# Performance work log

Hardware: AMD Instinct MI355X
Metric: run time of the kernel (lower is better)

The kernel has to match this reference:

```python
import jax, jax.numpy as jnp
import numpy as np

G, D, H, O = 8, 1024, 2048, 1024

def _xavier(key, shape):
    # xavier_normal_ on nn.Linear weight [out, in]: std = sqrt(2/(fan_in+fan_out))
    fan_out, fan_in = shape[-2], shape[-1]
    std = float(np.sqrt(2.0 / (fan_in + fan_out)))
    return jax.random.normal(key, shape, dtype=jnp.float32) * std

def setup_inputs() -> dict:
    key = jax.random.key(0)
    kx, kg, ku, kd = jax.random.split(key, 4)
    x = jax.random.normal(kx, (65536, D), dtype=jnp.float32)
    # weights stored per-group in nn.Linear layout [out, in]
    Wg = _xavier(kg, (G, H, D))
    Wu = _xavier(ku, (G, H, D))
    Wd = _xavier(kd, (G, O, H))
    return {"x": x, "Wg": Wg, "Wu": Wu, "Wd": Wd}

def reference(x, Wg, Wu, Wd):
    # x: [B*G, D] -> [B, G, D]
    xb = x.reshape(-1, G, D)
    gate = jnp.einsum('bgd,ghd->bgh', xb, Wg)   # [B, G, H]
    up = jnp.einsum('bgd,ghd->bgh', xb, Wu)     # [B, G, H]
    hidden = jax.nn.silu(gate) * up             # fused SwiGLU
    out = jnp.einsum('bgh,goh->bgo', hidden, Wd)  # [B, G, O]
    return out.reshape(-1, O)
```

## Files before the change

### kernel.cpp

```cpp
#include <hip/hip_runtime.h>


#define GN 8
#define DN 1024
#define HN 2048
#define ON 1024
#define BN 8192

typedef __attribute__((ext_vector_type(8))) short short8;
typedef __attribute__((ext_vector_type(4))) float f32x4;
typedef __attribute__((ext_vector_type(4))) unsigned int u32x4;

__device__ __forceinline__ void async16(const void* g, void* l) {
  __builtin_amdgcn_global_load_lds(
      (const __attribute__((address_space(1))) void*)g,
      (__attribute__((address_space(3))) void*)l, 16, 0, 0);
}

__device__ __forceinline__ unsigned short f2bf(float f) {
  unsigned int u = __float_as_uint(f);
  u += 0x7FFFu + ((u >> 16) & 1u);
  return (unsigned short)(u >> 16);
}

__global__ __launch_bounds__(256) void cvt_f32_bf16(
    const float* __restrict__ in, unsigned short* __restrict__ out, int n) {
  int t = blockIdx.x * 256 + threadIdx.x;
  int i = t * 8;
  if (i >= n) return;
  f32x4 a = *(const f32x4*)(in + i);
  f32x4 b = *(const f32x4*)(in + i + 4);
  u32x4 r;
  r.x = (unsigned)f2bf(a.x) | ((unsigned)f2bf(a.y) << 16);
  r.y = (unsigned)f2bf(a.z) | ((unsigned)f2bf(a.w) << 16);
  r.z = (unsigned)f2bf(b.x) | ((unsigned)f2bf(b.y) << 16);
  r.w = (unsigned)f2bf(b.z) | ((unsigned)f2bf(b.w) << 16);
  *(u32x4*)(out + i) = r;
}

__global__ __launch_bounds__(256, 2) void gemm1_swiglu(
    const unsigned short* __restrict__ Xb, const unsigned short* __restrict__ Wgb,
    const unsigned short* __restrict__ Wub, unsigned short* __restrict__ Hid) {
  const int g = blockIdx.z;
  const int m0 = blockIdx.x * 128;
  const int n0 = blockIdx.y * 64;
  const int tid = threadIdx.x;
  const int lane = tid & 63;
  const int w = tid >> 6;
  const int wm = w >> 1, wn = w & 1;

  __shared__ __align__(16) unsigned short lA[128 * 64];
  __shared__ __align__(16) unsigned short lG[64 * 64];
  __shared__ __align__(16) unsigned short lU[64 * 64];

  const int rl = lane >> 3;
  const int gc = (lane & 7) ^ rl;

  const unsigned short* aptr[4];
#pragma unroll
  for (int i = 0; i < 4; ++i) {
    int r = w * 32 + i * 8 + rl;
    aptr[i] = Xb + ((size_t)((m0 + r) * 8 + g)) * DN + gc * 8;
  }
  const unsigned short *gptr[2], *uptr[2];
#pragma unroll
  for (int i = 0; i < 2; ++i) {
    int r = w * 16 + i * 8 + rl;
    gptr[i] = Wgb + ((size_t)(g * HN + n0 + r)) * DN + gc * 8;
    uptr[i] = Wub + ((size_t)(g * HN + n0 + r)) * DN + gc * 8;
  }

  f32x4 accg[4][2], accu[4][2];
#pragma unroll
  for (int mi = 0; mi < 4; ++mi)
#pragma unroll
    for (int ni = 0; ni < 2; ++ni) {
      accg[mi][ni] = (f32x4)(0.0f);
      accu[mi][ni] = (f32x4)(0.0f);
    }

  for (int k0 = 0; k0 < DN; k0 += 64) {
#pragma unroll
    for (int i = 0; i < 4; ++i)
      async16(aptr[i] + k0, &lA[(w * 32 + i * 8) * 64]);
#pragma unroll
    for (int i = 0; i < 2; ++i) {
      async16(gptr[i] + k0, &lG[(w * 16 + i * 8) * 64]);
      async16(uptr[i] + k0, &lU[(w * 16 + i * 8) * 64]);
    }
    __syncthreads();

#pragma unroll
    for (int ks = 0; ks < 2; ++ks) {
      const int c = (lane >> 4) + ks * 4;
      short8 af[4], bg[2], bu[2];
#pragma unroll
      for (int mi = 0; mi < 4; ++mi) {
        int r = wm * 64 + mi * 16 + (lane & 15);
        af[mi] = *(const short8*)&lA[r * 64 + ((c ^ (r & 7)) * 8)];
      }
#pragma unroll
      for (int ni = 0; ni < 2; ++ni) {
        int r = wn * 32 + ni * 16 + (lane & 15);
        int off = r * 64 + ((c ^ (r & 7)) * 8);
        bg[ni] = *(const short8*)&lG[off];
        bu[ni] = *(const short8*)&lU[off];
      }
#pragma unroll
      for (int mi = 0; mi < 4; ++mi)
#pragma unroll
        for (int ni = 0; ni < 2; ++ni) {
          accg[mi][ni] = __builtin_amdgcn_mfma_f32_16x16x32_bf16(
              af[mi], bg[ni], accg[mi][ni], 0, 0, 0);
          accu[mi][ni] = __builtin_amdgcn_mfma_f32_16x16x32_bf16(
              af[mi], bu[ni], accu[mi][ni], 0, 0, 0);
        }
    }
    __syncthreads();
  }

  const int q = lane >> 4, cl = lane & 15;
#pragma unroll
  for (int mi = 0; mi < 4; ++mi)
#pragma unroll
    for (int ni = 0; ni < 2; ++ni) {
      int hcol = n0 + wn * 32 + ni * 16 + cl;
#pragma unroll
      for (int i = 0; i < 4; ++i) {
        int b = m0 + wm * 64 + mi * 16 + q * 4 + i;
        float gf = accg[mi][ni][i];
        float uf = accu[mi][ni][i];
        float hv = (gf / (1.0f + __expf(-gf))) * uf;
        Hid[((size_t)(b * 8 + g)) * HN + hcol] = f2bf(hv);
      }
    }
}

__global__ __launch_bounds__(256, 2) void gemm2_down(
    const unsigned short* __restrict__ Hid, const unsigned short* __restrict__ Wdb,
    float* __restrict__ Out) {
  const int g = blockIdx.z;
  const int m0 = blockIdx.x * 128;
  const int n0 = blockIdx.y * 128;
  const int tid = threadIdx.x;
  const int lane = tid & 63;
  const int w = tid >> 6;
  const int wm = w >> 1, wn = w & 1;

  __shared__ __align__(16) unsigned short lA[128 * 64];
  __shared__ __align__(16) unsigned short lB[128 * 64];

  const int rl = lane >> 3;
  const int gc = (lane & 7) ^ rl;

  const unsigned short *aptr[4], *bptr[4];
#pragma unroll
  for (int i = 0; i < 4; ++i) {
    int r = w * 32 + i * 8 + rl;
    aptr[i] = Hid + ((size_t)((m0 + r) * 8 + g)) * HN + gc * 8;
    bptr[i] = Wdb + ((size_t)(g * ON + n0 + r)) * HN + gc * 8;
  }

  f32x4 acc[4][4];
#pragma unroll
  for (int mi = 0; mi < 4; ++mi)
#pragma unroll
    for (int ni = 0; ni < 4; ++ni) acc[mi][ni] = (f32x4)(0.0f);

  for (int k0 = 0; k0 < HN; k0 += 64) {
#pragma unroll
    for (int i = 0; i < 4; ++i) {
      async16(aptr[i] + k0, &lA[(w * 32 + i * 8) * 64]);
      async16(bptr[i] + k0, &lB[(w * 32 + i * 8) * 64]);
    }
    __syncthreads();

#pragma unroll
    for (int ks = 0; ks < 2; ++ks) {
      const int c = (lane >> 4) + ks * 4;
      short8 af[4], bf[4];
#pragma unroll
      for (int mi = 0; mi < 4; ++mi) {
        int r = wm * 64 + mi * 16 + (lane & 15);
        af[mi] = *(const short8*)&lA[r * 64 + ((c ^ (r & 7)) * 8)];
      }
#pragma unroll
      for (int ni = 0; ni < 4; ++ni) {
        int r = wn * 64 + ni * 16 + (lane & 15);
        bf[ni] = *(const short8*)&lB[r * 64 + ((c ^ (r & 7)) * 8)];
      }
#pragma unroll
      for (int mi = 0; mi < 4; ++mi)
#pragma unroll
        for (int ni = 0; ni < 4; ++ni)
          acc[mi][ni] = __builtin_amdgcn_mfma_f32_16x16x32_bf16(
              af[mi], bf[ni], acc[mi][ni], 0, 0, 0);
    }
    __syncthreads();
  }

  const int q = lane >> 4, cl = lane & 15;
#pragma unroll
  for (int mi = 0; mi < 4; ++mi)
#pragma unroll
    for (int ni = 0; ni < 4; ++ni) {
      int o = n0 + wn * 64 + ni * 16 + cl;
#pragma unroll
      for (int i = 0; i < 4; ++i) {
        int b = m0 + wm * 64 + mi * 16 + q * 4 + i;
        Out[((size_t)(b * 8 + g)) * ON + o] = acc[mi][ni][i];
      }
    }
}

extern "C" void kernel_launch(void* const* d_in, const int* in_sizes, int n_in,
                              void* d_out, int out_size, void* d_ws, size_t ws_size,
                              hipStream_t stream) {
  const float* x  = (const float*)d_in[0];
  const float* Wg = (const float*)d_in[1];
  const float* Wu = (const float*)d_in[2];
  const float* Wd = (const float*)d_in[3];
  float* out = (float*)d_out;

  const int NX = 65536 * 1024;
  const int NW = GN * HN * DN;

  unsigned short* xb = (unsigned short*)d_ws;
  unsigned short* wg = xb + (size_t)NX;
  unsigned short* wu = wg + (size_t)NW;
  unsigned short* wd = wu + (size_t)NW;
  unsigned short* hid = wd + (size_t)NW;

  cvt_f32_bf16<<<NX / 8 / 256, 256, 0, stream>>>(x, xb, NX);
  cvt_f32_bf16<<<NW / 8 / 256, 256, 0, stream>>>(Wg, wg, NW);
  cvt_f32_bf16<<<NW / 8 / 256, 256, 0, stream>>>(Wu, wu, NW);
  cvt_f32_bf16<<<NW / 8 / 256, 256, 0, stream>>>(Wd, wd, NW);

  gemm1_swiglu<<<dim3(BN / 128, HN / 64, GN), 256, 0, stream>>>(xb, wg, wu, hid);

  gemm2_down<<<dim3(BN / 128, ON / 128, GN), 256, 0, stream>>>(hid, wd, out);
}
```

Before: 1.438 ms.

## Rewrite both GEMMs as 256-tile, 8-wave, multi-buffered pipelined MFMA kernels

Both grouped GEMM kernels move to 512-thread blocks with larger 256-row tiles (256x128 for gate/up, 256x256 for down) and a 128 KB dynamic-LDS four-slot buffer split into K halves. Async global-to-LDS loads are interleaved with MFMA phases under explicit vmcnt waits, barriers and raised wave priority. A 1D grid with an XCD-aware block swizzle improves L2 reuse. The aim is to hide load latency and raise arithmetic intensity per LDS byte, at the cost of more registers per thread and heavy reliance on fragile hand-tuned waitcnt accounting.

```diff
diff --git a/kernel.cpp b/kernel.cpp
--- a/kernel.cpp
+++ b/kernel.cpp
@@ -5,11 +5,13 @@
 #define DN 1024
 #define HN 2048
 #define ON 1024
-#define BN 8192
 
 typedef __attribute__((ext_vector_type(8))) short short8;
 typedef __attribute__((ext_vector_type(4))) float f32x4;
 typedef __attribute__((ext_vector_type(4))) unsigned int u32x4;
+
+#define SBAR() __builtin_amdgcn_sched_barrier(0)
+#define BARR() __builtin_amdgcn_s_barrier()
 
 __device__ __forceinline__ void async16(const void* g, void* l) {
   __builtin_amdgcn_global_load_lds(
@@ -38,177 +40,309 @@
   *(u32x4*)(out + i) = r;
 }
 
-__global__ __launch_bounds__(256, 2) void gemm1_swiglu(
+__global__ __launch_bounds__(512, 2) void gemm1_swiglu(
     const unsigned short* __restrict__ Xb, const unsigned short* __restrict__ Wgb,
     const unsigned short* __restrict__ Wub, unsigned short* __restrict__ Hid) {
-  const int g = blockIdx.z;
-  const int m0 = blockIdx.x * 128;
-  const int n0 = blockIdx.y * 64;
+  extern __shared__ unsigned short sm[];
+  unsigned short* sA = sm;
+  unsigned short* sG = sm + 32768;
+  unsigned short* sU = sm + 49152;
+
+  const int bid = blockIdx.x;
+  const int swz = (bid & 7) * 512 + (bid >> 3);
+  const int g = swz >> 9;
+  const int rem = swz & 511;
+  const int m0 = (rem >> 4) * 256;
+  const int n0 = (rem & 15) * 128;
+
   const int tid = threadIdx.x;
   const int lane = tid & 63;
   const int w = tid >> 6;
-  const int wm = w >> 1, wn = w & 1;
-
-  __shared__ __align__(16) unsigned short lA[128 * 64];
-  __shared__ __align__(16) unsigned short lG[64 * 64];
-  __shared__ __align__(16) unsigned short lU[64 * 64];
-
-  const int rl = lane >> 3;
-  const int gc = (lane & 7) ^ rl;
-
-  const unsigned short* aptr[4];
-#pragma unroll
-  for (int i = 0; i < 4; ++i) {
-    int r = w * 32 + i * 8 + rl;
-    aptr[i] = Xb + ((size_t)((m0 + r) * 8 + g)) * DN + gc * 8;
-  }
-  const unsigned short *gptr[2], *uptr[2];
-#pragma unroll
-  for (int i = 0; i < 2; ++i) {
-    int r = w * 16 + i * 8 + rl;
-    gptr[i] = Wgb + ((size_t)(g * HN + n0 + r)) * DN + gc * 8;
-    uptr[i] = Wub + ((size_t)(g * HN + n0 + r)) * DN + gc * 8;
-  }
-
-  f32x4 accg[4][2], accu[4][2];
-#pragma unroll
-  for (int mi = 0; mi < 4; ++mi)
+  const int wm = w >> 2, wn = w & 3;
+  const int fr = lane & 15, fc = lane >> 4;
+  const int sR = (fc + ((fr >> 1) & 3)) & 3;
+
+  const unsigned short* aSrc[2];
+  unsigned short* aDst[2];
+#pragma unroll
+  for (int j = 0; j < 2; ++j) {
+    int R = j * 128 + w * 16 + (lane >> 2);
+    int c = ((lane & 3) - ((R >> 1) & 3)) & 3;
+    aSrc[j] = Xb + ((size_t)((m0 + R) * 8 + g)) * DN + c * 8;
+    aDst[j] = &sA[(j * 128 + w * 16) * 32];
+  }
+  const unsigned short *gSrc, *uSrc;
+  unsigned short *gDst, *uDst;
+  {
+    int R = w * 16 + (lane >> 2);
+    int c = ((lane & 3) - ((R >> 1) & 3)) & 3;
+    gSrc = Wgb + ((size_t)(g * HN + n0 + R)) * DN + c * 8;
+    uSrc = Wub + ((size_t)(g * HN + n0 + R)) * DN + c * 8;
+    gDst = &sG[(w * 16) * 32];
+    uDst = &sU[(w * 16) * 32];
+  }
+
+  auto stageA = [&](int t, int kk) {
+    const int buf = (t & 1) * 2 + kk;
+    const int ko = t * 64 + kk * 32;
+#pragma unroll
+    for (int j = 0; j < 2; ++j) async16(aSrc[j] + ko, aDst[j] + buf * 8192);
+  };
+  auto stageB = [&](int t, int kk) {
+    const int buf = (t & 1) * 2 + kk;
+    const int ko = t * 64 + kk * 32;
+    async16(gSrc + ko, gDst + buf * 4096);
+    async16(uSrc + ko, uDst + buf * 4096);
+  };
+  auto readA = [&](int t, int kk, short8* a) {
+    const unsigned short* p =
+        sA + ((t & 1) * 2 + kk) * 8192 + (wm * 128 + fr) * 32 + sR * 8;
+#pragma unroll
+    for (int mi = 0; mi < 8; ++mi) a[mi] = *(const short8*)(p + mi * 512);
+  };
+  auto readB = [&](const unsigned short* base, int t, int kk, short8* b) {
+    const unsigned short* p =
+        base + ((t & 1) * 2 + kk) * 4096 + (wn * 32 + fr) * 32 + sR * 8;
+#pragma unroll
+    for (int ni = 0; ni < 2; ++ni) b[ni] = *(const short8*)(p + ni * 512);
+  };
+
+  f32x4 accg[8][2], accu[8][2];
+#pragma unroll
+  for (int mi = 0; mi < 8; ++mi)
 #pragma unroll
     for (int ni = 0; ni < 2; ++ni) {
       accg[mi][ni] = (f32x4)(0.0f);
       accu[mi][ni] = (f32x4)(0.0f);
     }
 
-  for (int k0 = 0; k0 < DN; k0 += 64) {
-#pragma unroll
-    for (int i = 0; i < 4; ++i)
-      async16(aptr[i] + k0, &lA[(w * 32 + i * 8) * 64]);
-#pragma unroll
-    for (int i = 0; i < 2; ++i) {
-      async16(gptr[i] + k0, &lG[(w * 16 + i * 8) * 64]);
-      async16(uptr[i] + k0, &lU[(w * 16 + i * 8) * 64]);
-    }
-    __syncthreads();
-
-#pragma unroll
-    for (int ks = 0; ks < 2; ++ks) {
-      const int c = (lane >> 4) + ks * 4;
-      short8 af[4], bg[2], bu[2];
-#pragma unroll
-      for (int mi = 0; mi < 4; ++mi) {
-        int r = wm * 64 + mi * 16 + (lane & 15);
-        af[mi] = *(const short8*)&lA[r * 64 + ((c ^ (r & 7)) * 8)];
-      }
-#pragma unroll
-      for (int ni = 0; ni < 2; ++ni) {
-        int r = wn * 32 + ni * 16 + (lane & 15);
-        int off = r * 64 + ((c ^ (r & 7)) * 8);
-        bg[ni] = *(const short8*)&lG[off];
-        bu[ni] = *(const short8*)&lU[off];
-      }
-#pragma unroll
-      for (int mi = 0; mi < 4; ++mi)
-#pragma unroll
-        for (int ni = 0; ni < 2; ++ni) {
-          accg[mi][ni] = __builtin_amdgcn_mfma_f32_16x16x32_bf16(
-              af[mi], bg[ni], accg[mi][ni], 0, 0, 0);
-          accu[mi][ni] = __builtin_amdgcn_mfma_f32_16x16x32_bf16(
-              af[mi], bu[ni], accu[mi][ni], 0, 0, 0);
-        }
-    }
-    __syncthreads();
+  auto mm16 = [&](const short8* a, const short8* b, f32x4(*acc)[2]) {
+    __builtin_amdgcn_s_setprio(1);
+#pragma unroll
+    for (int mi = 0; mi < 8; ++mi)
+#pragma unroll
+      for (int ni = 0; ni < 2; ++ni)
+        acc[mi][ni] = __builtin_amdgcn_mfma_f32_16x16x32_bf16(
+            a[mi], b[ni], acc[mi][ni], 0, 0, 0);
+    __builtin_amdgcn_s_setprio(0);
+  };
+
+  stageA(0, 0); stageB(0, 0); stageA(0, 1); stageB(0, 1);
+  stageA(1, 0); stageB(1, 0); stageA(1, 1);
+  asm volatile("s_waitcnt vmcnt(6)" ::: "memory");
+  SBAR(); BARR(); SBAR();
+
+  short8 af[8], bg[2], bu[2];
+  const int NIT = DN / 128;
+#pragma unroll 1
+  for (int i = 0; i < NIT; ++i) {
+    const int T = 2 * i;
+    const bool full = (i + 1 < NIT);
+    readA(T, 0, af); readB(sG, T, 0, bg);
+    stageB(T + 1, 1);
+    SBAR(); BARR(); SBAR();
+    mm16(af, bg, accg);
+    SBAR(); BARR(); SBAR();
+    readB(sU, T, 0, bu);
+    if (full) stageA(T + 2, 0);
+    SBAR(); BARR(); SBAR();
+    mm16(af, bu, accu);
+    SBAR(); BARR(); SBAR();
+    readA(T, 1, af); readB(sG, T, 1, bg);
+    if (full) stageB(T + 2, 0);
+    SBAR(); BARR(); SBAR();
+    mm16(af, bg, accg);
+    SBAR(); BARR(); SBAR();
+    readB(sU, T, 1, bu);
+    if (full) stageA(T + 2, 1);
+    SBAR(); BARR(); SBAR();
+    mm16(af, bu, accu);
+    if (full) { asm volatile("s_waitcnt vmcnt(6)" ::: "memory"); }
+    else      { asm volatile("s_waitcnt vmcnt(0)" ::: "memory"); }
+    SBAR(); BARR(); SBAR();
+    readA(T + 1, 0, af); readB(sG, T + 1, 0, bg);
+    if (full) stageB(T + 2, 1);
+    SBAR(); BARR(); SBAR();
+    mm16(af, bg, accg);
+    SBAR(); BARR(); SBAR();
+    readB(sU, T + 1, 0, bu);
+    if (full) stageA(T + 3, 0);
+    SBAR(); BARR(); SBAR();
+    mm16(af, bu, accu);
+    SBAR(); BARR(); SBAR();
+    readA(T + 1, 1, af); readB(sG, T + 1, 1, bg);
+    if (full) stageB(T + 3, 0);
+    SBAR(); BARR(); SBAR();
+    mm16(af, bg, accg);
+    SBAR(); BARR(); SBAR();
+    readB(sU, T + 1, 1, bu);
+    if (full) stageA(T + 3, 1);
+    SBAR(); BARR(); SBAR();
+    mm16(af, bu, accu);
+    if (full) { asm volatile("s_waitcnt vmcnt(6)" ::: "memory"); }
+    SBAR(); BARR(); SBAR();
   }
 
   const int q = lane >> 4, cl = lane & 15;
 #pragma unroll
-  for (int mi = 0; mi < 4; ++mi)
+  for (int mi = 0; mi < 8; ++mi)
 #pragma unroll
     for (int ni = 0; ni < 2; ++ni) {
       int hcol = n0 + wn * 32 + ni * 16 + cl;
 #pragma unroll
-      for (int i = 0; i < 4; ++i) {
-        int b = m0 + wm * 64 + mi * 16 + q * 4 + i;
-        float gf = accg[mi][ni][i];
-        float uf = accu[mi][ni][i];
+      for (int i2 = 0; i2 < 4; ++i2) {
+        int b = m0 + wm * 128 + mi * 16 + q * 4 + i2;
+        float gf = accg[mi][ni][i2];
+        float uf = accu[mi][ni][i2];
         float hv = (gf / (1.0f + __expf(-gf))) * uf;
         Hid[((size_t)(b * 8 + g)) * HN + hcol] = f2bf(hv);
       }
     }
 }
 
-__global__ __launch_bounds__(256, 2) void gemm2_down(
+__global__ __launch_bounds__(512, 2) void gemm2_down(
     const unsigned short* __restrict__ Hid, const unsigned short* __restrict__ Wdb,
     float* __restrict__ Out) {
-  const int g = blockIdx.z;
-  const int m0 = blockIdx.x * 128;
-  const int n0 = blockIdx.y * 128;
+  extern __shared__ unsigned short sm[];
+  unsigned short* sA = sm;
+  unsigned short* sB = sm + 32768;
+
+  const int bid = blockIdx.x;
+  const int swz = (bid & 7) * 128 + (bid >> 3);
+  const int g = swz >> 7;
+  const int rem = swz & 127;
+  const int m0 = (rem >> 2) * 256;
+  const int n0 = (rem & 3) * 256;
+
   const int tid = threadIdx.x;
   const int lane = tid & 63;
   const int w = tid >> 6;
-  const int wm = w >> 1, wn = w & 1;
-
-  __shared__ __align__(16) unsigned short lA[128 * 64];
-  __shared__ __align__(16) unsigned short lB[128 * 64];
-
-  const int rl = lane >> 3;
-  const int gc = (lane & 7) ^ rl;
-
-  const unsigned short *aptr[4], *bptr[4];
-#pragma unroll
-  for (int i = 0; i < 4; ++i) {
-    int r = w * 32 + i * 8 + rl;
-    aptr[i] = Hid + ((size_t)((m0 + r) * 8 + g)) * HN + gc * 8;
-    bptr[i] = Wdb + ((size_t)(g * ON + n0 + r)) * HN + gc * 8;
-  }
-
-  f32x4 acc[4][4];
-#pragma unroll
-  for (int mi = 0; mi < 4; ++mi)
+  const int wm = w >> 2, wn = w & 3;
+  const int fr = lane & 15, fc = lane >> 4;
+  const int sR = (fc + ((fr >> 1) & 3)) & 3;
+
+  const unsigned short* aSrc[2];
+  const unsigned short* bSrc[2];
+  unsigned short* aDst[2];
+  unsigned short* bDst[2];
+#pragma unroll
+  for (int j = 0; j < 2; ++j) {
+    int R = j * 128 + w * 16 + (lane >> 2);
+    int c = ((lane & 3) - ((R >> 1) & 3)) & 3;
+    aSrc[j] = Hid + ((size_t)((m0 + R) * 8 + g)) * HN + c * 8;
+    bSrc[j] = Wdb + ((size_t)(g * ON + n0 + R)) * HN + c * 8;
+    aDst[j] = &sA[(j * 128 + w * 16) * 32];
+    bDst[j] = &sB[(j * 128 + w * 16) * 32];
+  }
+
+  auto stageA = [&](int t, int kk) {
+    const int buf = (t & 1) * 2 + kk;
+    const int ko = t * 64 + kk * 32;
+#pragma unroll
+    for (int j = 0; j < 2; ++j) async16(aSrc[j] + ko, aDst[j] + buf * 8192);
+  };
+  auto stageB = [&](int t, int kk) {
+    const int buf = (t & 1) * 2 + kk;
+    const int ko = t * 64 + kk * 32;
+#pragma unroll
+    for (int j = 0; j < 2; ++j) async16(bSrc[j] + ko, bDst[j] + buf * 8192);
+  };
+  auto readA = [&](int t, int kk, short8* a) {
+    const unsigned short* p =
+        sA + ((t & 1) * 2 + kk) * 8192 + (wm * 128 + fr) * 32 + sR * 8;
+#pragma unroll
+    for (int mi = 0; mi < 8; ++mi) a[mi] = *(const short8*)(p + mi * 512);
+  };
+  auto readB = [&](int t, int kk, int nb, short8* b) {
+    const unsigned short* p =
+        sB + ((t & 1) * 2 + kk) * 8192 + (wn * 64 + nb * 16 + fr) * 32 + sR * 8;
+#pragma unroll
+    for (int nj = 0; nj < 2; ++nj) b[nj] = *(const short8*)(p + nj * 512);
+  };
+
+  f32x4 acc[8][4];
+#pragma unroll
+  for (int mi = 0; mi < 8; ++mi)
 #pragma unroll
     for (int ni = 0; ni < 4; ++ni) acc[mi][ni] = (f32x4)(0.0f);
 
-  for (int k0 = 0; k0 < HN; k0 += 64) {
-#pragma unroll
-    for (int i = 0; i < 4; ++i) {
-      async16(aptr[i] + k0, &lA[(w * 32 + i * 8) * 64]);
-      async16(bptr[i] + k0, &lB[(w * 32 + i * 8) * 64]);
-    }
-    __syncthreads();
-
-#pragma unroll
-    for (int ks = 0; ks < 2; ++ks) {
-      const int c = (lane >> 4) + ks * 4;
-      short8 af[4], bf[4];
-#pragma unroll
-      for (int mi = 0; mi < 4; ++mi) {
-        int r = wm * 64 + mi * 16 + (lane & 15);
-        af[mi] = *(const short8*)&lA[r * 64 + ((c ^ (r & 7)) * 8)];
-      }
-#pragma unroll
-      for (int ni = 0; ni < 4; ++ni) {
-        int r = wn * 64 + ni * 16 + (lane & 15);
-        bf[ni] = *(const short8*)&lB[r * 64 + ((c ^ (r & 7)) * 8)];
-      }
-#pragma unroll
-      for (int mi = 0; mi < 4; ++mi)
-#pragma unroll
-        for (int ni = 0; ni < 4; ++ni)
-          acc[mi][ni] = __builtin_amdgcn_mfma_f32_16x16x32_bf16(
-              af[mi], bf[ni], acc[mi][ni], 0, 0, 0);
-    }
-    __syncthreads();
+  auto mm16 = [&](const short8* a, const short8* b, int nb) {
+    __builtin_amdgcn_s_setprio(1);
+#pragma unroll
+    for (int mi = 0; mi < 8; ++mi)
+#pragma unroll
+      for (int nj = 0; nj < 2; ++nj)
+        acc[mi][nb + nj] = __builtin_amdgcn_mfma_f32_16x16x32_bf16(
+            a[mi], b[nj], acc[mi][nb + nj], 0, 0, 0);
+    __builtin_amdgcn_s_setprio(0);
+  };
+
+  stageA(0, 0); stageB(0, 0); stageA(0, 1); stageB(0, 1);
+  stageA(1, 0); stageB(1, 0); stageA(1, 1);
+  asm volatile("s_waitcnt vmcnt(6)" ::: "memory");
+  SBAR(); BARR(); SBAR();
+
+  short8 af[8], bf[2];
+  const int NIT = HN / 128;
+#pragma unroll 1
+  for (int i = 0; i < NIT; ++i) {
+    const int T = 2 * i;
+    const bool full = (i + 1 < NIT);
+    readA(T, 0, af); readB(T, 0, 0, bf);
+    stageB(T + 1, 1);
+    SBAR(); BARR(); SBAR();
+    mm16(af, bf, 0);
+    SBAR(); BARR(); SBAR();
+    readB(T, 0, 2, bf);
+    if (full) stageA(T + 2, 0);
+    SBAR(); BARR(); SBAR();
+    mm16(af, bf, 2);
+    SBAR(); BARR(); SBAR();
+    readA(T, 1, af); readB(T, 1, 0, bf);
+    if (full) stageB(T + 2, 0);
+    SBAR(); BARR(); SBAR();
+    mm16(af, bf, 0);
+    SBAR(); BARR(); SBAR();
+    readB(T, 1, 2, bf);
+    if (full) stageA(T + 2, 1);
+    SBAR(); BARR(); SBAR();
+    mm16(af, bf, 2);
+    if (full) { asm volatile("s_waitcnt vmcnt(6)" ::: "memory"); }
+    else      { asm volatile("s_waitcnt vmcnt(0)" ::: "memory"); }
+    SBAR(); BARR(); SBAR();
+    readA(T + 1, 0, af); readB(T + 1, 0, 0, bf);
+    if (full) stageB(T + 2, 1);
+    SBAR(); BARR(); SBAR();
+    mm16(af, bf, 0);
+    SBAR(); BARR(); SBAR();
+    readB(T + 1, 0, 2, bf);
+    if (full) stageA(T + 3, 0);
+    SBAR(); BARR(); SBAR();
+    mm16(af, bf, 2);
+    SBAR(); BARR(); SBAR();
+    readA(T + 1, 1, af); readB(T + 1, 1, 0, bf);
+    if (full) stageB(T + 3, 0);
+    SBAR(); BARR(); SBAR();
+    mm16(af, bf, 0);
+    SBAR(); BARR(); SBAR();
+    readB(T + 1, 1, 2, bf);
+    if (full) stageA(T + 3, 1);
+    SBAR(); BARR(); SBAR();
+    mm16(af, bf, 2);
+    if (full) { asm volatile("s_waitcnt vmcnt(6)" ::: "memory"); }
+    SBAR(); BARR(); SBAR();
   }
 
   const int q = lane >> 4, cl = lane & 15;
 #pragma unroll
-  for (int mi = 0; mi < 4; ++mi)
+  for (int mi = 0; mi < 8; ++mi)
 #pragma unroll
     for (int ni = 0; ni < 4; ++ni) {
       int o = n0 + wn * 64 + ni * 16 + cl;
 #pragma unroll
-      for (int i = 0; i < 4; ++i) {
-        int b = m0 + wm * 64 + mi * 16 + q * 4 + i;
-        Out[((size_t)(b * 8 + g)) * ON + o] = acc[mi][ni][i];
+      for (int i2 = 0; i2 < 4; ++i2) {
+        int b = m0 + wm * 128 + mi * 16 + q * 4 + i2;
+        Out[((size_t)(b * 8 + g)) * ON + o] = acc[mi][ni][i2];
       }
     }
 }
@@ -231,12 +365,20 @@
   unsigned short* wd = wu + (size_t)NW;
   unsigned short* hid = wd + (size_t)NW;
 
+  static bool once = false;
+  if (!once) {
+    hipFuncSetAttribute((const void*)gemm1_swiglu,
+                        hipFuncAttributeMaxDynamicSharedMemorySize, 131072);
+    hipFuncSetAttribute((const void*)gemm2_down,
+                        hipFuncAttributeMaxDynamicSharedMemorySize, 131072);
+    once = true;
+  }
+
   cvt_f32_bf16<<<NX / 8 / 256, 256, 0, stream>>>(x, xb, NX);
   cvt_f32_bf16<<<NW / 8 / 256, 256, 0, stream>>>(Wg, wg, NW);
   cvt_f32_bf16<<<NW / 8 / 256, 256, 0, stream>>>(Wu, wu, NW);
   cvt_f32_bf16<<<NW / 8 / 256, 256, 0, stream>>>(Wd, wd, NW);
 
-  gemm1_swiglu<<<dim3(BN / 128, HN / 64, GN), 256, 0, stream>>>(xb, wg, wu, hid);
-
-  gemm2_down<<<dim3(BN / 128, ON / 128, GN), 256, 0, stream>>>(hid, wd, out);
-}
+  gemm1_swiglu<<<dim3(4096), dim3(512), 131072, stream>>>(xb, wg, wu, hid);
+  gemm2_down<<<dim3(1024), dim3(512), 131072, stream>>>(hid, wd, out);
+}
```

Result: faster. 1.369 ms (-4.8%).
